# Kernel optimization log

Measured on AMD Instinct MI355X. Metric: run time of the kernel, lower is better.

Reference implementation:

```python
import jax, jax.numpy as jnp
import numpy as np

D = 1024        # input_dim
H = 4096        # hidden_dim (expert FFN width)
RH = H // 2     # router hidden
E = 8           # expert_count
TOP_K = 2
N = 4096        # tokens
LN_EPS = 1e-5


def setup_inputs() -> dict:
    key = jax.random.key(0)
    ks = jax.random.split(key, 12)
    s_d = 1.0 / np.sqrt(D)
    s_h = 1.0 / np.sqrt(H)
    s_rh = 1.0 / np.sqrt(RH)
    return {
        "x": jax.random.normal(ks[0], (N, D), jnp.float32),
        "ln_g": jnp.ones((D,), jnp.float32),
        "ln_b": jnp.zeros((D,), jnp.float32),
        # router: Linear(D, RH) -> ReLU -> Linear(RH, E)
        "rw1": jax.random.uniform(ks[1], (D, RH), jnp.float32, -s_d, s_d),
        "rb1": jax.random.uniform(ks[2], (RH,), jnp.float32, -s_d, s_d),
        "rw2": jax.random.uniform(ks[3], (RH, E), jnp.float32, -s_rh, s_rh),
        "rb2": jax.random.uniform(ks[4], (E,), jnp.float32, -s_rh, s_rh),
        # experts: E x (Linear(D, H) -> ReLU -> Linear(H, D)); dropout is identity in eval
        "ew1": jax.random.uniform(ks[5], (E, D, H), jnp.float32, -s_d, s_d),
        "eb1": jax.random.uniform(ks[6], (E, H), jnp.float32, -s_d, s_d),
        "ew2": jax.random.uniform(ks[7], (E, H, D), jnp.float32, -s_h, s_h),
        "eb2": jax.random.uniform(ks[8], (E, D), jnp.float32, -s_h, s_h),
    }


def reference(x, ln_g, ln_b, rw1, rb1, rw2, rb2, ew1, eb1, ew2, eb2):
    residual = x
    # LayerNorm
    mu = jnp.mean(x, axis=-1, keepdims=True)
    var = jnp.mean(jnp.square(x - mu), axis=-1, keepdims=True)
    xn = (x - mu) * jax.lax.rsqrt(var + LN_EPS) * ln_g + ln_b
    # Router MLP + softmax + top-k with renormalized gates
    logits = jax.nn.relu(xn @ rw1 + rb1) @ rw2 + rb2          # [N, E]
    probs = jax.nn.softmax(logits, axis=-1)
    vals, idx = jax.lax.top_k(probs, TOP_K)                    # [N, K]
    vals = vals / jnp.sum(vals, axis=-1, keepdims=True)
    # combine weights per expert: [N, E]
    combine = jnp.sum(jax.nn.one_hot(idx, E, dtype=vals.dtype) * vals[..., None], axis=1)
    # dense grouped expert FFN: h [E, N, H], y [E, N, D]
    h = jax.nn.relu(jnp.einsum("nd,edh->enh", xn, ew1) + eb1[:, None, :])
    y = jnp.einsum("enh,ehd->end", h, ew2) + eb2[:, None, :]
    out = residual + jnp.einsum("end,ne->nd", y, combine)
    return out
```

## Files before the change

kernel.cpp:

```cpp
#include <hip/hip_runtime.h>
#include <stdint.h>

#define D_    1024
#define H_    4096
#define RH_   2048
#define E_    8
#define N_    4096
#define NK_   8192
#define MT_MAX 71
#define DELTA_MARGIN 1e-4f
#define FIX_CAP 256

typedef __bf16 bf16x8 __attribute__((ext_vector_type(8)));
typedef float  f32x4  __attribute__((ext_vector_type(4)));


__device__ __forceinline__ unsigned short f2bf(float f) {
  union { float f; unsigned u; } v; v.f = f;
  unsigned r = v.u + 0x7fffu + ((v.u >> 16) & 1u);
  return (unsigned short)(r >> 16);
}
__device__ __forceinline__ float bf2f(unsigned short h) {
  union { unsigned u; float f; } v; v.u = ((unsigned)h) << 16;
  return v.f;
}

#define GLOAD16(gp, lp) \
  __builtin_amdgcn_global_load_lds((__attribute__((address_space(1))) void*)(void*)(gp), \
                                   (__attribute__((address_space(3))) void*)(lp), 16, 0, 0)

__global__ __launch_bounds__(256) void k_transpose(const float* __restrict__ in,
                                                   unsigned short* __restrict__ outH,
                                                   unsigned short* __restrict__ outL,
                                                   int R, int C) {
  __shared__ float t[32][33];
  const int b = blockIdx.z;
  const int c0 = blockIdx.x * 32, r0 = blockIdx.y * 32;
  const int lx = threadIdx.x & 31, ly = threadIdx.x >> 5;
  const long inB = (long)R * C;
  #pragma unroll
  for (int i = 0; i < 4; i++) {
    int r = r0 + ly + i * 8;
    t[ly + i * 8][lx] = in[b * inB + (long)r * C + c0 + lx];
  }
  __syncthreads();
  #pragma unroll
  for (int i = 0; i < 4; i++) {
    int c = c0 + ly + i * 8;
    float v = t[lx][ly + i * 8];
    unsigned short h = f2bf(v);
    long oi = b * inB + (long)c * R + r0 + lx;
    outH[oi] = h;
    if (outL) outL[oi] = f2bf(v - bf2f(h));
  }
}

__global__ __launch_bounds__(256) void k_layernorm(const float* __restrict__ x,
                                                   const float* __restrict__ g,
                                                   const float* __restrict__ b,
                                                   unsigned short* __restrict__ xnh,
                                                   unsigned short* __restrict__ xnl) {
  __shared__ float red[4];
  const int n = blockIdx.x, tid = threadIdx.x;
  float4 v = ((const float4*)(x + (long)n * D_))[tid];
  float s = v.x + v.y + v.z + v.w;
  #pragma unroll
  for (int o = 32; o >= 1; o >>= 1) s += __shfl_xor(s, o, 64);
  if ((tid & 63) == 0) red[tid >> 6] = s;
  __syncthreads();
  float mean = (red[0] + red[1] + red[2] + red[3]) * (1.f / D_);
  __syncthreads();
  float d0 = v.x - mean, d1 = v.y - mean, d2 = v.z - mean, d3 = v.w - mean;
  float ss = d0 * d0 + d1 * d1 + d2 * d2 + d3 * d3;
  #pragma unroll
  for (int o = 32; o >= 1; o >>= 1) ss += __shfl_xor(ss, o, 64);
  if ((tid & 63) == 0) red[tid >> 6] = ss;
  __syncthreads();
  float rstd = rsqrtf((red[0] + red[1] + red[2] + red[3]) * (1.f / D_) + 1e-5f);
  float4 gg = ((const float4*)g)[tid];
  float4 bb = ((const float4*)b)[tid];
  float xn0 = d0 * rstd * gg.x + bb.x;
  float xn1 = d1 * rstd * gg.y + bb.y;
  float xn2 = d2 * rstd * gg.z + bb.z;
  float xn3 = d3 * rstd * gg.w + bb.w;
  unsigned short h0 = f2bf(xn0), h1 = f2bf(xn1), h2 = f2bf(xn2), h3 = f2bf(xn3);
  ((ushort4*)xnh)[(long)n * 256 + tid] = make_ushort4(h0, h1, h2, h3);
  ((ushort4*)xnl)[(long)n * 256 + tid] = make_ushort4(
      f2bf(xn0 - bf2f(h0)), f2bf(xn1 - bf2f(h1)),
      f2bf(xn2 - bf2f(h2)), f2bf(xn3 - bf2f(h3)));
}

__global__ void k_init(int* ctl) { if (threadIdx.x < 36) ctl[threadIdx.x] = 0; }

__global__ __launch_bounds__(256) void k_router_gemm(const unsigned short* __restrict__ xh,
                                                     const unsigned short* __restrict__ xl,
                                                     const unsigned short* __restrict__ bhT,
                                                     const unsigned short* __restrict__ blT,
                                                     const float* __restrict__ rb1,
                                                     float* __restrict__ h_r) {
  __shared__ __align__(16) unsigned short Ah[128 * 32], Al[128 * 32], Bh[128 * 32], Bl[128 * 32];
  const int tid = threadIdx.x, lane = tid & 63, wid = tid >> 6;
  const int m0 = blockIdx.x * 128, n0 = blockIdx.y * 128;
  const int wm = wid >> 1, wn = wid & 1;
  const int seg0 = wid * 2;
  const int srow = lane >> 2;
  const int scol = (lane & 3) * 8;
  const long a0 = (long)(m0 + seg0 * 16 + srow) * D_ + scol;
  const long a1 = a0 + 16 * D_;
  const long b0 = (long)(n0 + seg0 * 16 + srow) * D_ + scol;
  const long b1 = b0 + 16 * D_;
  const int rl = lane & 15, kh8 = (lane >> 4) * 8;
  f32x4 acc[4][4];
  #pragma unroll
  for (int i = 0; i < 4; i++)
    #pragma unroll
    for (int j = 0; j < 4; j++) acc[i][j] = 0.f;

  for (int k0 = 0; k0 < D_; k0 += 32) {
    GLOAD16(xh + a0 + k0, Ah + seg0 * 512);
    GLOAD16(xh + a1 + k0, Ah + seg0 * 512 + 512);
    GLOAD16(xl + a0 + k0, Al + seg0 * 512);
    GLOAD16(xl + a1 + k0, Al + seg0 * 512 + 512);
    GLOAD16(bhT + b0 + k0, Bh + seg0 * 512);
    GLOAD16(bhT + b1 + k0, Bh + seg0 * 512 + 512);
    GLOAD16(blT + b0 + k0, Bl + seg0 * 512);
    GLOAD16(blT + b1 + k0, Bl + seg0 * 512 + 512);
    __syncthreads();
    bf16x8 bhf[4], blf[4];
    #pragma unroll
    for (int ni = 0; ni < 4; ni++) {
      int r = (wn * 64 + ni * 16 + rl) * 32 + kh8;
      bhf[ni] = *(const bf16x8*)(Bh + r);
      blf[ni] = *(const bf16x8*)(Bl + r);
    }
    #pragma unroll
    for (int mi = 0; mi < 4; mi++) {
      int r = (wm * 64 + mi * 16 + rl) * 32 + kh8;
      bf16x8 ah = *(const bf16x8*)(Ah + r);
      bf16x8 al = *(const bf16x8*)(Al + r);
      #pragma unroll
      for (int ni = 0; ni < 4; ni++) {
        acc[mi][ni] = __builtin_amdgcn_mfma_f32_16x16x32_bf16(ah, bhf[ni], acc[mi][ni], 0, 0, 0);
        acc[mi][ni] = __builtin_amdgcn_mfma_f32_16x16x32_bf16(ah, blf[ni], acc[mi][ni], 0, 0, 0);
        acc[mi][ni] = __builtin_amdgcn_mfma_f32_16x16x32_bf16(al, bhf[ni], acc[mi][ni], 0, 0, 0);
      }
    }
    __syncthreads();
  }
  const int rg4 = (lane >> 4) * 4;
  #pragma unroll
  for (int ni = 0; ni < 4; ni++) {
    int col = n0 + wn * 64 + ni * 16 + rl;
    float bias = rb1[col];
    #pragma unroll
    for (int mi = 0; mi < 4; mi++) {
      int row = m0 + wm * 64 + mi * 16 + rg4;
      #pragma unroll
      for (int r = 0; r < 4; r++) {
        float v = acc[mi][ni][r] + bias;
        h_r[(long)(row + r) * RH_ + col] = v > 0.f ? v : 0.f;
      }
    }
  }
}

__global__ __launch_bounds__(256) void k_logits_top2(const float* __restrict__ h_r,
                                                     const float* __restrict__ rw2,
                                                     const float* __restrict__ rb2,
                                                     int* __restrict__ sel, float* __restrict__ gate,
                                                     int* __restrict__ marked, int* __restrict__ mcount) {
  const int lane = threadIdx.x & 63, wid = threadIdx.x >> 6;
  const int n = blockIdx.x * 4 + wid;
  float p[8] = {0, 0, 0, 0, 0, 0, 0, 0};
  const float* hr = h_r + (long)n * RH_;
  for (int i = 0; i < RH_ / 64; i++) {
    int c = i * 64 + lane;
    float v = hr[c];
    float4 wa = ((const float4*)(rw2 + c * 8))[0];
    float4 wb = ((const float4*)(rw2 + c * 8))[1];
    p[0] += v * wa.x; p[1] += v * wa.y; p[2] += v * wa.z; p[3] += v * wa.w;
    p[4] += v * wb.x; p[5] += v * wb.y; p[6] += v * wb.z; p[7] += v * wb.w;
  }
  #pragma unroll
  for (int e = 0; e < 8; e++)
    #pragma unroll
    for (int s = 32; s >= 1; s >>= 1) p[e] += __shfl_xor(p[e], s, 64);
  if (lane == 0) {
    float l1 = -1e30f, l2 = -1e30f, l3 = -1e30f; int e1 = 0, e2 = 0;
    #pragma unroll
    for (int e = 0; e < 8; e++) {
      float v = p[e] + rb2[e];
      if (v > l1)      { l3 = l2; l2 = l1; e2 = e1; l1 = v; e1 = e; }
      else if (v > l2) { l3 = l2; l2 = v; e2 = e; }
      else if (v > l3) { l3 = v; }
    }
    float g1 = 1.f / (1.f + expf(l2 - l1));
    sel[n * 2] = e1; sel[n * 2 + 1] = e2;
    gate[n * 2] = g1; gate[n * 2 + 1] = 1.f - g1;
    if (l2 - l3 < DELTA_MARGIN) { int i = atomicAdd(mcount, 1); marked[i] = n; }
  }
}

__global__ __launch_bounds__(256) void k_fixup1(const float* __restrict__ x,
                                                const float* __restrict__ ln_g, const float* __restrict__ ln_b,
                                                const float* __restrict__ rw1, const float* __restrict__ rb1,
                                                const int* __restrict__ marked, const int* __restrict__ mcount,
                                                double* __restrict__ hsbuf) {
  __shared__ float xs[D_];
  __shared__ float redf[4];
  __shared__ double part[64][5];
  const int tid = threadIdx.x;
  int cnt = *mcount; if (cnt > FIX_CAP) cnt = FIX_CAP;
  const int blkTok = blockIdx.x >> 5;
  const int chunk  = blockIdx.x & 31;
  for (int mi = blkTok; mi < cnt; mi += FIX_CAP) {
    const int n = marked[mi];
    float4 v = ((const float4*)(x + (long)n * D_))[tid];
    float s = v.x + v.y + v.z + v.w;
    #pragma unroll
    for (int o = 32; o >= 1; o >>= 1) s += __shfl_xor(s, o, 64);
    if ((tid & 63) == 0) redf[tid >> 6] = s;
    __syncthreads();
    float mean = (redf[0] + redf[1] + redf[2] + redf[3]) * (1.f / D_);
    __syncthreads();
    float d0 = v.x - mean, d1 = v.y - mean, d2 = v.z - mean, d3 = v.w - mean;
    float ss = d0 * d0 + d1 * d1 + d2 * d2 + d3 * d3;
    #pragma unroll
    for (int o = 32; o >= 1; o >>= 1) ss += __shfl_xor(ss, o, 64);
    if ((tid & 63) == 0) redf[tid >> 6] = ss;
    __syncthreads();
    float rstd = rsqrtf((redf[0] + redf[1] + redf[2] + redf[3]) * (1.f / D_) + 1e-5f);
    float4 gg = ((const float4*)ln_g)[tid];
    float4 bb = ((const float4*)ln_b)[tid];
    xs[tid * 4 + 0] = d0 * rstd * gg.x + bb.x;
    xs[tid * 4 + 1] = d1 * rstd * gg.y + bb.y;
    xs[tid * 4 + 2] = d2 * rstd * gg.z + bb.z;
    xs[tid * 4 + 3] = d3 * rstd * gg.w + bb.w;
    __syncthreads();
    const int lcol = tid & 63, prt = tid >> 6;
    const int col = chunk * 64 + lcol;
    const float* rp = rw1 + (long)(prt * 256) * RH_ + col;
    const float* xp = xs + prt * 256;
    double a0 = 0, a1 = 0, a2 = 0, a3 = 0;
    #pragma unroll 4
    for (int d = 0; d < 256; d += 4) {
      float w0 = rp[(long)(d + 0) * RH_];
      float w1 = rp[(long)(d + 1) * RH_];
      float w2 = rp[(long)(d + 2) * RH_];
      float w3 = rp[(long)(d + 3) * RH_];
      a0 += (double)xp[d + 0] * (double)w0;
      a1 += (double)xp[d + 1] * (double)w1;
      a2 += (double)xp[d + 2] * (double)w2;
      a3 += (double)xp[d + 3] * (double)w3;
    }
    part[lcol][prt] = (a0 + a1) + (a2 + a3);
    __syncthreads();
    if (tid < 64) {
      double a = (part[tid][0] + part[tid][1]) + (part[tid][2] + part[tid][3])
               + (double)rb1[chunk * 64 + tid];
      hsbuf[(long)mi * RH_ + chunk * 64 + tid] = a > 0.0 ? a : 0.0;
    }
    __syncthreads();
  }
}

__global__ __launch_bounds__(256) void k_fixup2(const double* __restrict__ hsbuf,
                                                const float* __restrict__ rw2, const float* __restrict__ rb2,
                                                const int* __restrict__ marked, const int* __restrict__ mcount,
                                                int* __restrict__ sel, float* __restrict__ gate) {
  __shared__ double red2[256];
  const int tid = threadIdx.x;
  int cnt = *mcount; if (cnt > FIX_CAP) cnt = FIX_CAP;
  for (int mi = blockIdx.x; mi < cnt; mi += gridDim.x) {
    const int n = marked[mi];
    const double* hs = hsbuf + (long)mi * RH_;
    const int e = tid & 7, ch = tid >> 3;
    double pp = 0.0;
    for (int c = ch * 64; c < ch * 64 + 64; c++) pp += hs[c] * (double)rw2[c * 8 + e];
    red2[tid] = pp;
    __syncthreads();
    if (tid < 128) red2[tid] += red2[tid + 128];
    __syncthreads();
    if (tid < 64) red2[tid] += red2[tid + 64];
    __syncthreads();
    if (tid < 32) red2[tid] += red2[tid + 32];
    __syncthreads();
    if (tid < 16) red2[tid] += red2[tid + 16];
    __syncthreads();
    if (tid < 8) red2[tid] += red2[tid + 8];
    __syncthreads();
    if (tid == 0) {
      double l1 = -1e300, l2 = -1e300; int e1 = 0, e2 = 0;
      for (int ee = 0; ee < 8; ee++) {
        double vv = red2[ee] + (double)rb2[ee];
        if (vv > l1)      { l2 = l1; e2 = e1; l1 = vv; e1 = ee; }
        else if (vv > l2) { l2 = vv; e2 = ee; }
      }
      double g1 = 1.0 / (1.0 + exp(l2 - l1));
      sel[n * 2] = e1; sel[n * 2 + 1] = e2;
      gate[n * 2] = (float)g1; gate[n * 2 + 1] = (float)(1.0 - g1);
    }
    __syncthreads();
  }
}

__global__ void k_count(const int* __restrict__ sel, int* ctl) {
  int n = blockIdx.x * 256 + threadIdx.x;
  if (n >= N_) return;
  atomicAdd(&ctl[sel[n * 2]], 1);
  atomicAdd(&ctl[sel[n * 2 + 1]], 1);
}
__global__ void k_offsets(int* ctl) {
  if (threadIdx.x == 0 && blockIdx.x == 0) {
    int t = 0, tt = 0;
    for (int e = 0; e < 8; e++) {
      ctl[8 + e] = t; ctl[17 + e] = tt; ctl[26 + e] = t;
      t += ctl[e]; tt += (ctl[e] + 127) >> 7;
    }
    ctl[16] = t; ctl[25] = tt;
  }
}
__global__ void k_scatter(const int* __restrict__ sel, int* ctl,
                          int* __restrict__ perm, int* __restrict__ pos) {
  int n = blockIdx.x * 256 + threadIdx.x;
  if (n >= N_) return;
  #pragma unroll
  for (int k = 0; k < 2; k++) {
    int e = sel[n * 2 + k];
    int p = atomicAdd(&ctl[26 + e], 1);
    perm[p] = n;
    pos[n * 2 + k] = p;
  }
}

template <int KD, bool GATHER, bool RELU_BF16, bool MTFAST>
__global__ __launch_bounds__(256) void k_gemm_expert4(const unsigned short* __restrict__ A,
                                                      const unsigned short* __restrict__ BT,
                                                      const float* __restrict__ bias,
                                                      const int* __restrict__ ctl,
                                                      const int* __restrict__ perm,
                                                      unsigned short* __restrict__ outBF,
                                                      float* __restrict__ outF32, int NB) {
  const int* cnt = ctl; const int* off = ctl + 8; const int* toff = ctl + 17;
  const int NX = gridDim.x, MT = gridDim.y;
  const int nwg = NX * MT;
  const int F = blockIdx.y * NX + blockIdx.x;
  const int q = nwg >> 3, r8 = nwg & 7;
  const int xcd = F & 7, j = F >> 3;
  const int L = (xcd < r8 ? xcd * (q + 1) : r8 * (q + 1) + (xcd - r8) * q) + j;
  int mt, nt;
  if (MTFAST) { mt = L % MT; nt = L / MT; }
  else        { nt = L % NX; mt = L / NX; }
  if (mt >= toff[8]) return;
  int e = 0;
  #pragma unroll
  for (int i = 0; i < 7; i++) if (toff[i + 1] <= mt) e = i + 1;
  const int ltile = mt - toff[e];
  const int g0 = off[e] + ltile * 128;
  int vrows = cnt[e] - ltile * 128; if (vrows > 128) vrows = 128;
  const int n0 = nt * 128;

  __shared__ __align__(16) unsigned short At[2][128 * 64];
  __shared__ __align__(16) unsigned short Bt[2][128 * 64];
  const int tid = threadIdx.x, lane = tid & 63, wid = tid >> 6;
  const int l8 = lane >> 3, s8 = lane & 7;
  const int ksw = (s8 ^ l8) * 8;

  long aa[4], bb[4];
  const long bbase = (long)e * NB * KD;
  const int gmax = off[e] + cnt[e] - 1;
  #pragma unroll
  for (int i = 0; i < 4; i++) {
    int row = wid * 32 + i * 8 + l8;
    long ar;
    if constexpr (GATHER) {
      int g = g0 + row;
      ar = perm[g <= gmax ? g : gmax];
    } else {
      ar = g0 + row;
    }
    aa[i] = ar * (long)KD + ksw;
    bb[i] = bbase + (long)(n0 + row) * KD + ksw;
  }

  const int wm = wid >> 1, wn = wid & 1;
  const int rl = lane & 15, g4 = lane >> 4;
  int sA[2], sB[2];
  #pragma unroll
  for (int kk = 0; kk < 2; kk++) {
    sA[kk] = ((kk * 4 + g4) ^ (rl & 7)) * 8;
    sB[kk] = sA[kk];
  }

  f32x4 acc[4][4];
  #pragma unroll
  for (int i = 0; i < 4; i++)
    #pragma unroll
    for (int jj = 0; jj < 4; jj++) acc[i][jj] = 0.f;

  auto stage = [&](int bi, int k0) {
    #pragma unroll
    for (int i = 0; i < 4; i++) {
      GLOAD16(A + aa[i] + k0, &At[bi][(wid * 32 + i * 8) * 64]);
      GLOAD16(BT + bb[i] + k0, &Bt[bi][(wid * 32 + i * 8) * 64]);
    }
  };
  auto compute = [&](int bi) {
    #pragma unroll
    for (int kk = 0; kk < 2; kk++) {
      bf16x8 bfr[4];
      #pragma unroll
      for (int ni = 0; ni < 4; ni++)
        bfr[ni] = *(const bf16x8*)(&Bt[bi][(wn * 64 + ni * 16 + rl) * 64 + sB[kk]]);
      #pragma unroll
      for (int mi = 0; mi < 4; mi++) {
        bf16x8 af = *(const bf16x8*)(&At[bi][(wm * 64 + mi * 16 + rl) * 64 + sA[kk]]);
        #pragma unroll
        for (int ni = 0; ni < 4; ni++)
          acc[mi][ni] = __builtin_amdgcn_mfma_f32_16x16x32_bf16(af, bfr[ni], acc[mi][ni], 0, 0, 0);
      }
    }
  };

  constexpr int NT = KD / 64;
  stage(0, 0);
  __syncthreads();
  int cur = 0;
  for (int t = 0; t < NT - 1; ++t) {
    stage(cur ^ 1, (t + 1) * 64);
    compute(cur);
    __syncthreads();
    cur ^= 1;
  }
  compute(cur);

  const int rg4 = (lane >> 4) * 4;
  #pragma unroll
  for (int ni = 0; ni < 4; ni++) {
    int col = n0 + wn * 64 + ni * 16 + rl;
    float bv = bias[(long)e * NB + col];
    #pragma unroll
    for (int mi = 0; mi < 4; mi++) {
      int lrow = wm * 64 + mi * 16 + rg4;
      #pragma unroll
      for (int r = 0; r < 4; r++) {
        if (lrow + r < vrows) {
          float v = acc[mi][ni][r] + bv;
          long idx = (long)(g0 + lrow + r) * NB + col;
          if constexpr (RELU_BF16) outBF[idx] = f2bf(v > 0.f ? v : 0.f);
          else outF32[idx] = v;
        }
      }
    }
  }
}

__global__ __launch_bounds__(256) void k_combine(const float* __restrict__ x,
                                                 const float* __restrict__ y_buf,
                                                 const int* __restrict__ pos,
                                                 const float* __restrict__ gate,
                                                 float* __restrict__ out) {
  const int n = blockIdx.x, t = threadIdx.x;
  const float g0 = gate[n * 2], g1 = gate[n * 2 + 1];
  const long p0 = pos[n * 2], p1 = pos[n * 2 + 1];
  float4 xv = ((const float4*)(x + (long)n * D_))[t];
  float4 a = ((const float4*)(y_buf + p0 * D_))[t];
  float4 b = ((const float4*)(y_buf + p1 * D_))[t];
  float4 o;
  o.x = xv.x + g0 * a.x + g1 * b.x;
  o.y = xv.y + g0 * a.y + g1 * b.y;
  o.z = xv.z + g0 * a.z + g1 * b.z;
  o.w = xv.w + g0 * a.w + g1 * b.w;
  ((float4*)(out + (long)n * D_))[t] = o;
}

extern "C" void kernel_launch(void* const* d_in, const int* in_sizes, int n_in,
                              void* d_out, int out_size, void* d_ws, size_t ws_size,
                              hipStream_t stream) {
  const float* x    = (const float*)d_in[0];
  const float* ln_g = (const float*)d_in[1];
  const float* ln_b = (const float*)d_in[2];
  const float* rw1  = (const float*)d_in[3];
  const float* rb1  = (const float*)d_in[4];
  const float* rw2  = (const float*)d_in[5];
  const float* rb2  = (const float*)d_in[6];
  const float* ew1  = (const float*)d_in[7];
  const float* eb1  = (const float*)d_in[8];
  const float* ew2  = (const float*)d_in[9];
  const float* eb2  = (const float*)d_in[10];
  float* out = (float*)d_out;

  char* w = (char*)d_ws;
  size_t off = 0;
  auto alloc = [&](size_t bytes) -> char* {
    char* p = w + off;
    off += (bytes + 255) & ~(size_t)255;
    return p;
  };
  unsigned short* ew1T  = (unsigned short*)alloc((size_t)E_ * H_ * D_ * 2);
  unsigned short* ew2T  = (unsigned short*)alloc((size_t)E_ * D_ * H_ * 2);
  unsigned short* rw1hT = (unsigned short*)alloc((size_t)RH_ * D_ * 2);
  unsigned short* rw1lT = (unsigned short*)alloc((size_t)RH_ * D_ * 2);
  unsigned short* xnh   = (unsigned short*)alloc((size_t)N_ * D_ * 2);
  unsigned short* xnl   = (unsigned short*)alloc((size_t)N_ * D_ * 2);
  float*          h_r   = (float*)alloc((size_t)N_ * RH_ * 4);
  unsigned short* h_buf = (unsigned short*)alloc((size_t)(NK_ + 128) * H_ * 2);
  float*          y_buf = (float*)alloc((size_t)(NK_ + 128) * D_ * 4);
  double*         hsbuf = (double*)alloc((size_t)FIX_CAP * RH_ * 8);
  int*   sel    = (int*)alloc((size_t)N_ * 2 * 4);
  float* gate   = (float*)alloc((size_t)N_ * 2 * 4);
  int*   marked = (int*)alloc((size_t)N_ * 4);
  int*   perm   = (int*)alloc((size_t)NK_ * 4);
  int*   pos    = (int*)alloc((size_t)N_ * 2 * 4);
  int*   ctl    = (int*)alloc(64 * 4);

  k_transpose<<<dim3(H_ / 32, D_ / 32, E_), 256, 0, stream>>>(ew1, ew1T, nullptr, D_, H_);
  k_transpose<<<dim3(D_ / 32, H_ / 32, E_), 256, 0, stream>>>(ew2, ew2T, nullptr, H_, D_);
  k_transpose<<<dim3(RH_ / 32, D_ / 32, 1), 256, 0, stream>>>(rw1, rw1hT, rw1lT, D_, RH_);
  k_layernorm<<<N_, 256, 0, stream>>>(x, ln_g, ln_b, xnh, xnl);
  k_init<<<1, 64, 0, stream>>>(ctl);
  k_router_gemm<<<dim3(N_ / 128, RH_ / 128), 256, 0, stream>>>(xnh, xnl, rw1hT, rw1lT, rb1, h_r);
  k_logits_top2<<<N_ / 4, 256, 0, stream>>>(h_r, rw2, rb2, sel, gate, marked, ctl + 34);
  k_fixup1<<<FIX_CAP * 32, 256, 0, stream>>>(x, ln_g, ln_b, rw1, rb1, marked, ctl + 34, hsbuf);
  k_fixup2<<<64, 256, 0, stream>>>(hsbuf, rw2, rb2, marked, ctl + 34, sel, gate);
  k_count<<<N_ / 256, 256, 0, stream>>>(sel, ctl);
  k_offsets<<<1, 1, 0, stream>>>(ctl);
  k_scatter<<<N_ / 256, 256, 0, stream>>>(sel, ctl, perm, pos);
  k_gemm_expert4<D_, true, true, true><<<dim3(H_ / 128, MT_MAX), 256, 0, stream>>>(
      xnh, ew1T, eb1, ctl, perm, h_buf, nullptr, H_);
  k_gemm_expert4<H_, false, false, false><<<dim3(D_ / 128, MT_MAX), 256, 0, stream>>>(
      h_buf, ew2T, eb2, ctl, perm, nullptr, y_buf, D_);
  k_combine<<<N_, 256, 0, stream>>>(x, y_buf, pos, gate, out);

  (void)in_sizes; (void)n_in; (void)out_size; (void)ws_size;
}
```

Before: 617.2 us.

## Issue expert GEMM loads two tiles ahead and widen transpose tiles to 64x64

The expert GEMM main loop now prefetches two K-tiles before computing. It waits with a partial vmcnt so the next tile's global-to-LDS loads stay in flight during the MFMA work, and it refills the just-consumed buffer after a barrier. This is meant to hide global load latency that the old single-stage-ahead loop with full syncthreads exposed. The weight transpose kernel moves to 64x64 tiles with 16 elements per thread and vectorized ushort4 stores, to cut launch count and widen the writes. The transpose uses a larger LDS tile, and the manual waitcnt logic depends on the exact number of loads issued per stage.

```diff
diff --git a/kernel.cpp b/kernel.cpp
--- a/kernel.cpp
+++ b/kernel.cpp
@@ -33,25 +33,33 @@
                                                    unsigned short* __restrict__ outH,
                                                    unsigned short* __restrict__ outL,
                                                    int R, int C) {
-  __shared__ float t[32][33];
+  __shared__ float t[64][65];
   const int b = blockIdx.z;
-  const int c0 = blockIdx.x * 32, r0 = blockIdx.y * 32;
-  const int lx = threadIdx.x & 31, ly = threadIdx.x >> 5;
+  const int c0 = blockIdx.x * 64, r0 = blockIdx.y * 64;
+  const int lx = threadIdx.x & 63, ly = threadIdx.x >> 6;
   const long inB = (long)R * C;
-  #pragma unroll
-  for (int i = 0; i < 4; i++) {
-    int r = r0 + ly + i * 8;
-    t[ly + i * 8][lx] = in[b * inB + (long)r * C + c0 + lx];
-  }
+  const float* ip = in + b * inB + (long)r0 * C + c0 + lx;
+  #pragma unroll
+  for (int i = 0; i < 16; i++)
+    t[ly + i * 4][lx] = ip[(long)(ly + i * 4) * C];
   __syncthreads();
-  #pragma unroll
-  for (int i = 0; i < 4; i++) {
-    int c = c0 + ly + i * 8;
-    float v = t[lx][ly + i * 8];
-    unsigned short h = f2bf(v);
-    long oi = b * inB + (long)c * R + r0 + lx;
-    outH[oi] = h;
-    if (outL) outL[oi] = f2bf(v - bf2f(h));
+  const int wy = threadIdx.x >> 2;
+  const int wx = (threadIdx.x & 3) * 16;
+  const int c = c0 + wy;
+  const long ob = b * inB + (long)c * R + r0 + wx;
+  unsigned short h[16];
+  #pragma unroll
+  for (int j = 0; j < 16; j++) h[j] = f2bf(t[wx + j][wy]);
+  #pragma unroll
+  for (int j = 0; j < 4; j++)
+    *(ushort4*)&outH[ob + j * 4] = make_ushort4(h[j*4], h[j*4+1], h[j*4+2], h[j*4+3]);
+  if (outL) {
+    unsigned short l[16];
+    #pragma unroll
+    for (int j = 0; j < 16; j++) l[j] = f2bf(t[wx + j][wy] - bf2f(h[j]));
+    #pragma unroll
+    for (int j = 0; j < 4; j++)
+      *(ushort4*)&outL[ob + j * 4] = make_ushort4(l[j*4], l[j*4+1], l[j*4+2], l[j*4+3]);
   }
 }
 
@@ -334,7 +342,7 @@
 }
 
 template <int KD, bool GATHER, bool RELU_BF16, bool MTFAST>
-__global__ __launch_bounds__(256) void k_gemm_expert4(const unsigned short* __restrict__ A,
+__global__ __launch_bounds__(256) void k_gemm_expert5(const unsigned short* __restrict__ A,
                                                       const unsigned short* __restrict__ BT,
                                                       const float* __restrict__ bias,
                                                       const int* __restrict__ ctl,
@@ -385,12 +393,10 @@
 
   const int wm = wid >> 1, wn = wid & 1;
   const int rl = lane & 15, g4 = lane >> 4;
-  int sA[2], sB[2];
-  #pragma unroll
-  for (int kk = 0; kk < 2; kk++) {
+  int sA[2];
+  #pragma unroll
+  for (int kk = 0; kk < 2; kk++)
     sA[kk] = ((kk * 4 + g4) ^ (rl & 7)) * 8;
-    sB[kk] = sA[kk];
-  }
 
   f32x4 acc[4][4];
   #pragma unroll
@@ -411,7 +417,7 @@
       bf16x8 bfr[4];
       #pragma unroll
       for (int ni = 0; ni < 4; ni++)
-        bfr[ni] = *(const bf16x8*)(&Bt[bi][(wn * 64 + ni * 16 + rl) * 64 + sB[kk]]);
+        bfr[ni] = *(const bf16x8*)(&Bt[bi][(wn * 64 + ni * 16 + rl) * 64 + sA[kk]]);
       #pragma unroll
       for (int mi = 0; mi < 4; mi++) {
         bf16x8 af = *(const bf16x8*)(&At[bi][(wm * 64 + mi * 16 + rl) * 64 + sA[kk]]);
@@ -424,14 +430,32 @@
 
   constexpr int NT = KD / 64;
   stage(0, 0);
-  __syncthreads();
+  stage(1, 64);
   int cur = 0;
-  for (int t = 0; t < NT - 1; ++t) {
-    stage(cur ^ 1, (t + 1) * 64);
+  #pragma unroll 1
+  for (int t = 0; t < NT - 2; ++t) {
+    asm volatile("s_waitcnt vmcnt(8)" ::: "memory");
+    __builtin_amdgcn_sched_barrier(0);
+    __builtin_amdgcn_s_barrier();
+    asm volatile("" ::: "memory");
     compute(cur);
-    __syncthreads();
+    asm volatile("" ::: "memory");
+    __builtin_amdgcn_s_barrier();
+    stage(cur, (t + 2) * 64);
     cur ^= 1;
   }
+  asm volatile("s_waitcnt vmcnt(8)" ::: "memory");
+  __builtin_amdgcn_sched_barrier(0);
+  __builtin_amdgcn_s_barrier();
+  asm volatile("" ::: "memory");
+  compute(cur);
+  asm volatile("" ::: "memory");
+  __builtin_amdgcn_s_barrier();
+  cur ^= 1;
+  asm volatile("s_waitcnt vmcnt(0)" ::: "memory");
+  __builtin_amdgcn_sched_barrier(0);
+  __builtin_amdgcn_s_barrier();
+  asm volatile("" ::: "memory");
   compute(cur);
 
   const int rg4 = (lane >> 4) * 4;
@@ -514,9 +538,9 @@
   int*   pos    = (int*)alloc((size_t)N_ * 2 * 4);
   int*   ctl    = (int*)alloc(64 * 4);
 
-  k_transpose<<<dim3(H_ / 32, D_ / 32, E_), 256, 0, stream>>>(ew1, ew1T, nullptr, D_, H_);
-  k_transpose<<<dim3(D_ / 32, H_ / 32, E_), 256, 0, stream>>>(ew2, ew2T, nullptr, H_, D_);
-  k_transpose<<<dim3(RH_ / 32, D_ / 32, 1), 256, 0, stream>>>(rw1, rw1hT, rw1lT, D_, RH_);
+  k_transpose<<<dim3(H_ / 64, D_ / 64, E_), 256, 0, stream>>>(ew1, ew1T, nullptr, D_, H_);
+  k_transpose<<<dim3(D_ / 64, H_ / 64, E_), 256, 0, stream>>>(ew2, ew2T, nullptr, H_, D_);
+  k_transpose<<<dim3(RH_ / 64, D_ / 64, 1), 256, 0, stream>>>(rw1, rw1hT, rw1lT, D_, RH_);
   k_layernorm<<<N_, 256, 0, stream>>>(x, ln_g, ln_b, xnh, xnl);
   k_init<<<1, 64, 0, stream>>>(ctl);
   k_router_gemm<<<dim3(N_ / 128, RH_ / 128), 256, 0, stream>>>(xnh, xnl, rw1hT, rw1lT, rb1, h_r);
@@ -526,9 +550,9 @@
   k_count<<<N_ / 256, 256, 0, stream>>>(sel, ctl);
   k_offsets<<<1, 1, 0, stream>>>(ctl);
   k_scatter<<<N_ / 256, 256, 0, stream>>>(sel, ctl, perm, pos);
-  k_gemm_expert4<D_, true, true, true><<<dim3(H_ / 128, MT_MAX), 256, 0, stream>>>(
+  k_gemm_expert5<D_, true, true, true><<<dim3(H_ / 128, MT_MAX), 256, 0, stream>>>(
       xnh, ew1T, eb1, ctl, perm, h_buf, nullptr, H_);
-  k_gemm_expert4<H_, false, false, false><<<dim3(D_ / 128, MT_MAX), 256, 0, stream>>>(
+  k_gemm_expert5<H_, false, false, false><<<dim3(D_ / 128, MT_MAX), 256, 0, stream>>>(
       h_buf, ew2T, eb2, ctl, perm, nullptr, y_buf, D_);
   k_combine<<<N_, 256, 0, stream>>>(x, y_buf, pos, gate, out);
 
```

After: 584.6 us. 1.06x faster.
